# Performance work log

Measured on AMD Instinct MI355X. Metric: run time of the kernel, lower is better.

The kernel has to match this reference:

```python
import jax, jax.numpy as jnp
import numpy as np

B, S, D, DFF = 4, 2048, 1024, 4096
EPS = 1e-5


def layernorm(x, gamma, beta):
    mu = jnp.mean(x, axis=-1, keepdims=True)
    var = jnp.var(x, axis=-1, keepdims=True)
    return (x - mu) * jax.lax.rsqrt(var + EPS) * gamma + beta


def attention(Q, K, V, causal):
    d_k = Q.shape[-1]
    scores = jnp.einsum('bqd,bkd->bqk', Q, K) / jnp.sqrt(jnp.asarray(d_k, Q.dtype))
    if causal:
        q_len, k_len = scores.shape[-2], scores.shape[-1]
        mask = jnp.tril(jnp.ones((q_len, k_len), dtype=bool))
        scores = jnp.where(mask[None], scores, jnp.asarray(-jnp.inf, scores.dtype))
    w = jax.nn.softmax(scores, axis=-1)
    return jnp.einsum('bqk,bkd->bqd', w, V)


def setup_inputs() -> dict:
    key = jax.random.key(0)
    ks = jax.random.split(key, 12)
    sd = 0.02
    return {
        'y': jax.random.normal(ks[0], (B, S, D), jnp.float32),
        'Z': jax.random.normal(ks[1], (B, S, D), jnp.float32),
        'w1': jax.random.normal(ks[2], (D, DFF), jnp.float32) * sd,
        'b1': jnp.zeros((DFF,), jnp.float32),
        'w2': jax.random.normal(ks[3], (DFF, D), jnp.float32) * sd,
        'b2': jnp.zeros((D,), jnp.float32),
        'g1': jnp.ones((D,), jnp.float32), 'beta1': jnp.zeros((D,), jnp.float32),
        'g2': jnp.ones((D,), jnp.float32), 'beta2': jnp.zeros((D,), jnp.float32),
        'g3': jnp.ones((D,), jnp.float32), 'beta3': jnp.zeros((D,), jnp.float32),
    }


def reference(y, Z, w1, b1, w2, b2, g1, beta1, g2, beta2, g3, beta3):
    # masked (causal) self-attention, single head over full d_model
    sa = attention(y, y, y, causal=True)
    y = layernorm(y + sa, g1, beta1)
    # cross-attention to encoder memory Z
    ca = attention(y, Z, Z, causal=False)
    y = layernorm(y + ca, g2, beta2)
    # position-wise FFN
    h = jax.nn.relu(jnp.einsum('bsd,df->bsf', y, w1) + b1)
    ff = jnp.einsum('bsf,fd->bsd', h, w2) + b2
    y = layernorm(y + ff, g3, beta3)
    return y
```

## Files before the change

kernel.cpp:

```cpp
#include <hip/hip_runtime.h>
#include <hip/hip_bf16.h>


#define Bb 4
#define Ss 2048
#define Dd 1024
#define Ff 4096

typedef __attribute__((ext_vector_type(4))) float f32x4;
typedef __attribute__((ext_vector_type(8))) short bf16x8;
typedef __attribute__((ext_vector_type(8))) unsigned short u16x8;
typedef __attribute__((ext_vector_type(4))) unsigned short u16x4;

__device__ __forceinline__ unsigned short f2bf(float f) {
  unsigned u = __float_as_uint(f);
  u += 0x7FFFu + ((u >> 16) & 1u);
  return (unsigned short)(u >> 16);
}

__device__ __forceinline__ void gload_lds16(const void* g, void* l) {
  __builtin_amdgcn_global_load_lds((const __attribute__((address_space(1))) void*)g,
                                   (__attribute__((address_space(3))) void*)l, 16, 0, 0);
}

__device__ __forceinline__ int xcd8(int orig, int n) {
  int q = n >> 3, r = n & 7;
  int x = orig & 7;
  int base = x < r ? x * (q + 1) : r * (q + 1) + (x - r) * q;
  return base + (orig >> 3);
}

__global__ __launch_bounds__(256) void k_transpose_cast(const float* __restrict__ in,
                                                        unsigned short* __restrict__ outT,
                                                        unsigned short* __restrict__ outR,
                                                        int R, int C) {
  __shared__ float t[32][33];
  size_t bo = (size_t)blockIdx.z * R * C;
  const float* pin = in + bo;
  unsigned short* poutT = outT + bo;
  unsigned short* poutR = outR ? outR + bo : nullptr;
  int c0 = blockIdx.x * 32, r0 = blockIdx.y * 32;
  int tx = threadIdx.x, ty = threadIdx.y;
#pragma unroll
  for (int i = 0; i < 4; i++) {
    float v = pin[(size_t)(r0 + ty + i * 8) * C + c0 + tx];
    t[ty + i * 8][tx] = v;
    if (poutR) poutR[(size_t)(r0 + ty + i * 8) * C + c0 + tx] = f2bf(v);
  }
  __syncthreads();
#pragma unroll
  for (int i = 0; i < 4; i++)
    poutT[(size_t)(c0 + ty + i * 8) * R + r0 + tx] = f2bf(t[tx][ty + i * 8]);
}

#define BAR() __builtin_amdgcn_s_barrier()
#define PRIO1() __builtin_amdgcn_s_setprio(1)
#define PRIO0() __builtin_amdgcn_s_setprio(0)

#define LDA8(arr, mh, bo)                                                       \
  {                                                                             \
    _Pragma("unroll") for (int j_ = 0; j_ < QM; ++j_) {                         \
      _Pragma("unroll") for (int kh_ = 0; kh_ < 2; ++kh_) {                     \
        arr[j_][kh_] =                                                          \
            *(const bf16x8*)(lds + (bo) + ((mh)*QM + j_) * 2048 + aof[kh_]);    \
      }                                                                         \
    }                                                                           \
  }

#define LDB8(arr, nh, bo)                                                       \
  {                                                                             \
    _Pragma("unroll") for (int n_ = 0; n_ < 2; ++n_) {                          \
      _Pragma("unroll") for (int kh_ = 0; kh_ < 2; ++kh_) {                     \
        arr[n_][kh_] =                                                          \
            *(const bf16x8*)(lds + (bo) + ((nh)*2 + n_) * 2048 + bof[kh_]);     \
      }                                                                         \
    }                                                                           \
  }

#define MMQ(aarr, barr, mh, nh)                                                 \
  {                                                                             \
    _Pragma("unroll") for (int j_ = 0; j_ < QM; ++j_) {                         \
      _Pragma("unroll") for (int n_ = 0; n_ < 2; ++n_) {                        \
        _Pragma("unroll") for (int kh_ = 0; kh_ < 2; ++kh_) {                   \
          acc[(mh)*QM + j_][(nh)*2 + n_] = __builtin_amdgcn_mfma_f32_16x16x32_bf16( \
              aarr[j_][kh_], barr[n_][kh_], acc[(mh)*QM + j_][(nh)*2 + n_], 0, 0, 0); \
        }                                                                       \
      }                                                                         \
    }                                                                           \
  }

#define VMCNT()                                                                 \
  {                                                                             \
    if constexpr (NVM == 6) asm volatile("s_waitcnt vmcnt(6)" ::: "memory");    \
    else asm volatile("s_waitcnt vmcnt(4)" ::: "memory");                       \
  }

template <int BMt, int EPI, bool CAUSAL, bool KCAP>
__global__ __launch_bounds__(512) void k_gemm8(
    const unsigned short* __restrict__ Ag, const unsigned short* __restrict__ Bg,
    float* __restrict__ Cf, unsigned short* __restrict__ Cb,
    const float* __restrict__ bias, int K, int lda, int ldb, int ldc,
    long bsA, long bsB, long bsC, float scale) {
  constexpr int BNt = 256;
  constexpr int WMS = BMt / 2;
  constexpr int MR = WMS / 16;
  constexpr int QM = MR / 2;
  constexpr int LA = BMt / 128;
  constexpr int NVM = 2 * LA + 2;
  constexpr int ABYTES = BMt * 128;
  constexpr int BBYTES = BNt * 128;
  __shared__ alignas(16) char lds[2 * ABYTES + 2 * BBYTES];

  int i0, j0;
  if (CAUSAL) {
    int t = xcd8(blockIdx.x, gridDim.x);
    int ti = (int)((sqrtf(8.f * t + 1.f) - 1.f) * 0.5f);
    while ((ti + 1) * (ti + 2) / 2 <= t) ++ti;
    while (ti * (ti + 1) / 2 > t) --ti;
    i0 = ti * BMt;
    j0 = (t - ti * (ti + 1) / 2) * BNt;
  } else {
    int lin = xcd8(blockIdx.y * gridDim.x + blockIdx.x, gridDim.x * gridDim.y);
    i0 = (lin / gridDim.x) * BMt;
    j0 = (lin % gridDim.x) * BNt;
  }
  int bz = blockIdx.z;
  Ag += (size_t)bz * bsA;
  Bg += (size_t)bz * bsB;

  int nk = K / 64;
  if (KCAP) {
    int cap = i0 / 64 + BMt / 64;
    nk = nk < cap ? nk : cap;
  }
  const int niter = nk / 2;

  const int tid = threadIdx.x;
  const int w = tid >> 6, lane = tid & 63;
  const int wr = w >> 2, wc = w & 3;

  const int srow = (w << 3) + (lane >> 3);
  const int bcs = (lane & 7) ^ (lane >> 3);
  const unsigned short* As = Ag + (size_t)(i0 + srow) * lda + bcs * 8;
  const unsigned short* Bs = Bg + (size_t)(j0 + srow) * ldb + bcs * 8;
  char* ldsAw = lds + w * 1024;
  char* ldsBw = lds + 2 * ABYTES + w * 1024;

  auto stA = [&](int kt, int hf) {
    int ks = kt < nk ? kt : nk - 1;
#pragma unroll
    for (int l = 0; l < LA; ++l)
      gload_lds16(As + (size_t)(hf * (BMt / 2) + l * 64) * lda + ks * 64,
                  ldsAw + (kt & 1) * ABYTES + hf * (BMt / 2) * 128 + l * 8192);
  };
  auto stB = [&](int kt, int hf) {
    int ks = kt < nk ? kt : nk - 1;
#pragma unroll
    for (int l = 0; l < 2; ++l)
      gload_lds16(Bs + (size_t)(hf * 128 + l * 64) * ldb + ks * 64,
                  ldsBw + (kt & 1) * BBYTES + hf * 128 * 128 + l * 8192);
  };

  const int fr = lane & 15, kq = lane >> 4;
  const int rA = wr * WMS + fr;
  const int rB = wc * 64 + fr;
  unsigned aof[2], bof[2];
  aof[0] = rA * 128 + ((kq ^ (rA & 7)) << 4);
  aof[1] = rA * 128 + (((kq + 4) ^ (rA & 7)) << 4);
  bof[0] = 2 * ABYTES + rB * 128 + ((kq ^ (rB & 7)) << 4);
  bof[1] = 2 * ABYTES + rB * 128 + (((kq + 4) ^ (rB & 7)) << 4);
  constexpr int A0 = 0, A1 = ABYTES, B0 = 0, B1 = BBYTES;

  f32x4 acc[MR][4];
#pragma unroll
  for (int m = 0; m < MR; ++m)
#pragma unroll
    for (int n = 0; n < 4; ++n) acc[m][n] = (f32x4){0.f, 0.f, 0.f, 0.f};

  bf16x8 a0[QM][2], a1[QM][2], b0[2][2], b1[2][2];

  stA(0, 0); stA(0, 1); stB(0, 0); stB(0, 1);
  stA(1, 0); stA(1, 1); stB(1, 0);
  VMCNT();
  BAR();

  for (int t = 0; t < niter; ++t) {
    const int ka = 2 * t + 2, kb = 2 * t + 3;
    LDA8(a0, 0, A0); LDB8(b0, 0, B0);
    stB(2 * t + 1, 1);
    BAR(); PRIO1(); MMQ(a0, b0, 0, 0); PRIO0(); BAR();
    LDA8(a1, 1, A0);
    BAR(); PRIO1(); MMQ(a1, b0, 1, 0); PRIO0(); BAR();
    LDB8(b1, 1, B0);
    stA(ka, 0);
    BAR(); PRIO1(); MMQ(a1, b1, 1, 1); PRIO0(); BAR();
    stA(ka, 1); stB(ka, 0);
    VMCNT();
    BAR(); PRIO1(); MMQ(a0, b1, 0, 1); PRIO0(); BAR();
    LDA8(a0, 0, A1); LDB8(b0, 0, B1);
    stB(ka, 1);
    BAR(); PRIO1(); MMQ(a0, b0, 0, 0); PRIO0(); BAR();
    LDA8(a1, 1, A1);
    BAR(); PRIO1(); MMQ(a1, b0, 1, 0); PRIO0(); BAR();
    LDB8(b1, 1, B1);
    stA(kb, 0);
    BAR(); PRIO1(); MMQ(a1, b1, 1, 1); PRIO0(); BAR();
    stA(kb, 1); stB(kb, 0);
    VMCNT();
    BAR(); PRIO1(); MMQ(a0, b1, 0, 1); PRIO0(); BAR();
  }

  const int colb = j0 + wc * 64 + fr;
  const int rowb = i0 + wr * WMS + (kq << 2);
  const size_t cb = (size_t)bz * bsC;
#pragma unroll
  for (int m = 0; m < MR; ++m) {
#pragma unroll
    for (int r = 0; r < 4; ++r) {
      size_t ro = cb + (size_t)(rowb + m * 16 + r) * ldc;
#pragma unroll
      for (int n = 0; n < 4; ++n) {
        float v = acc[m][n][r];
        int col = colb + n * 16;
        if (EPI == 0) Cf[ro + col] = v * scale;
        else if (EPI == 1) Cf[ro + col] = v;
        else if (EPI == 2) Cb[ro + col] = f2bf(fmaxf(v + bias[col], 0.f));
        else Cf[ro + col] = v + bias[col];
      }
    }
  }
}

template <bool CAUSAL>
__global__ __launch_bounds__(256) void k_softmax(float* __restrict__ scores) {
  int row = blockIdx.x;
  int i = row & (Ss - 1);
  float* src = scores + (size_t)row * Ss;
  unsigned short* dst = (unsigned short*)src;
  int nv = CAUSAL ? i + 1 : Ss;
  int t = threadIdx.x;
  int w = t >> 6, lane = t & 63;
  float v[8];
  float mx = -1e30f;
#pragma unroll
  for (int k = 0; k < 8; k++) {
    int j = t + k * 256;
    v[k] = (j < nv) ? src[j] : -1e30f;
    mx = fmaxf(mx, v[k]);
  }
#pragma unroll
  for (int o = 32; o; o >>= 1) mx = fmaxf(mx, __shfl_xor(mx, o));
  __shared__ float red[8];
  if (lane == 0) red[w] = mx;
  __syncthreads();
  mx = fmaxf(fmaxf(red[0], red[1]), fmaxf(red[2], red[3]));
  float sum = 0.f;
#pragma unroll
  for (int k = 0; k < 8; k++) {
    int j = t + k * 256;
    float e = (j < nv) ? __expf(v[k] - mx) : 0.f;
    v[k] = e;
    sum += e;
  }
#pragma unroll
  for (int o = 32; o; o >>= 1) sum += __shfl_xor(sum, o);
  if (lane == 0) red[4 + w] = sum;
  __syncthreads();
  sum = red[4] + red[5] + red[6] + red[7];
  float inv = 1.f / sum;
#pragma unroll
  for (int k = 0; k < 8; k++) {
    int j = t + k * 256;
    dst[j] = f2bf(v[k] * inv);
  }
}

__global__ __launch_bounds__(256) void k_add_ln(const float* __restrict__ a,
                                                const float* __restrict__ b,
                                                const float* __restrict__ g,
                                                const float* __restrict__ be,
                                                float* __restrict__ outf,
                                                unsigned short* __restrict__ outb) {
  int row = blockIdx.x;
  size_t o = (size_t)row * Dd;
  int t = threadIdx.x;
  f32x4 xa = *(const f32x4*)(a + o + t * 4);
  f32x4 xb = *(const f32x4*)(b + o + t * 4);
  f32x4 x = xa + xb;
  float s = x[0] + x[1] + x[2] + x[3];
  float q = x[0] * x[0] + x[1] * x[1] + x[2] * x[2] + x[3] * x[3];
  int w = t >> 6, lane = t & 63;
#pragma unroll
  for (int of = 32; of; of >>= 1) {
    s += __shfl_xor(s, of);
    q += __shfl_xor(q, of);
  }
  __shared__ float red[8];
  if (lane == 0) {
    red[w] = s;
    red[4 + w] = q;
  }
  __syncthreads();
  s = red[0] + red[1] + red[2] + red[3];
  q = red[4] + red[5] + red[6] + red[7];
  float mean = s * (1.f / Dd);
  float var = q * (1.f / Dd) - mean * mean;
  float rstd = rsqrtf(var + 1e-5f);
  f32x4 gv = *(const f32x4*)(g + t * 4);
  f32x4 bv = *(const f32x4*)(be + t * 4);
  f32x4 y;
#pragma unroll
  for (int k = 0; k < 4; k++) y[k] = (x[k] - mean) * rstd * gv[k] + bv[k];
  *(f32x4*)(outf + o + t * 4) = y;
  if (outb) {
    u16x4 r;
    r[0] = f2bf(y[0]); r[1] = f2bf(y[1]); r[2] = f2bf(y[2]); r[3] = f2bf(y[3]);
    *(u16x4*)(outb + o + t * 4) = r;
  }
}

extern "C" void kernel_launch(void* const* d_in, const int* in_sizes, int n_in, void* d_out,
                              int out_size, void* d_ws, size_t ws_size, hipStream_t stream) {
  (void)in_sizes; (void)n_in; (void)out_size; (void)ws_size;
  const float* y   = (const float*)d_in[0];
  const float* Z   = (const float*)d_in[1];
  const float* w1  = (const float*)d_in[2];
  const float* b1  = (const float*)d_in[3];
  const float* w2  = (const float*)d_in[4];
  const float* b2  = (const float*)d_in[5];
  const float* g1  = (const float*)d_in[6];
  const float* be1 = (const float*)d_in[7];
  const float* g2  = (const float*)d_in[8];
  const float* be2 = (const float*)d_in[9];
  const float* g3  = (const float*)d_in[10];
  const float* be3 = (const float*)d_in[11];
  float* out = (float*)d_out;

  char* ws = (char*)d_ws;
  const size_t MB = 1024ull * 1024ull;
  unsigned short* T   = (unsigned short*)(ws);
  unsigned short* Zbf = (unsigned short*)(ws + 16 * MB);
  unsigned short* ybf = (unsigned short*)(ws + 32 * MB);
  unsigned short* w1t = (unsigned short*)(ws + 48 * MB);
  unsigned short* w2t = (unsigned short*)(ws + 56 * MB);
  float* sc           = (float*)(ws + 64 * MB);
  unsigned short* h   = (unsigned short*)(ws + 64 * MB);
  float* res          = (float*)(ws + 128 * MB);
  float* attn         = (float*)d_out;

  dim3 b256(256), b512(512);
  const float scl = 1.f / 32.f;

  k_transpose_cast<<<dim3(Dd / 32, Ss / 32, Bb), dim3(32, 8), 0, stream>>>(y, T, ybf, Ss, Dd);
  k_gemm8<256, 0, true, false><<<dim3(36, 1, Bb), b512, 0, stream>>>(
      ybf, ybf, sc, nullptr, nullptr, Dd, Dd, Dd, Ss, (long)Ss * Dd, (long)Ss * Dd,
      (long)Ss * Ss, scl);
  k_softmax<true><<<dim3(Bb * Ss), b256, 0, stream>>>(sc);
  k_gemm8<128, 1, false, true><<<dim3(Dd / 256, Ss / 128, Bb), b512, 0, stream>>>(
      (const unsigned short*)sc, T, attn, nullptr, nullptr, Ss, 2 * Ss, Ss, Dd,
      2L * Ss * Ss, (long)Dd * Ss, (long)Ss * Dd, 1.f);
  k_add_ln<<<dim3(Bb * Ss), b256, 0, stream>>>(y, attn, g1, be1, res, ybf);

  k_transpose_cast<<<dim3(Dd / 32, Ss / 32, Bb), dim3(32, 8), 0, stream>>>(Z, T, Zbf, Ss, Dd);
  k_gemm8<256, 0, false, false><<<dim3(Ss / 256, Ss / 256, Bb), b512, 0, stream>>>(
      ybf, Zbf, sc, nullptr, nullptr, Dd, Dd, Dd, Ss, (long)Ss * Dd, (long)Ss * Dd,
      (long)Ss * Ss, scl);
  k_softmax<false><<<dim3(Bb * Ss), b256, 0, stream>>>(sc);
  k_gemm8<128, 1, false, false><<<dim3(Dd / 256, Ss / 128, Bb), b512, 0, stream>>>(
      (const unsigned short*)sc, T, attn, nullptr, nullptr, Ss, 2 * Ss, Ss, Dd,
      2L * Ss * Ss, (long)Dd * Ss, (long)Ss * Dd, 1.f);
  k_add_ln<<<dim3(Bb * Ss), b256, 0, stream>>>(res, attn, g2, be2, res, ybf);

  k_transpose_cast<<<dim3(Ff / 32, Dd / 32, 1), dim3(32, 8), 0, stream>>>(w1, w1t, nullptr, Dd, Ff);
  k_transpose_cast<<<dim3(Dd / 32, Ff / 32, 1), dim3(32, 8), 0, stream>>>(w2, w2t, nullptr, Ff, Dd);
  k_gemm8<256, 2, false, false><<<dim3(Ff / 256, (Bb * Ss) / 256, 1), b512, 0, stream>>>(
      ybf, w1t, nullptr, h, b1, Dd, Dd, Dd, Ff, 0L, 0L, 0L, 1.f);
  k_gemm8<128, 3, false, false><<<dim3(Dd / 256, (Bb * Ss) / 128, 1), b512, 0, stream>>>(
      h, w2t, attn, nullptr, b2, Ff, Ff, Ff, Dd, 0L, 0L, 0L, 1.f);
  k_add_ln<<<dim3(Bb * Ss), b256, 0, stream>>>(res, attn, g3, be3, out, nullptr);
}
```

Measured before the change: 406.5 us.

## Write attention scores as bf16, vectorize softmax, split GEMM into 256/128-row kernels

The score GEMMs now write bf16 scores directly instead of fp32. The softmax reads and writes those bf16 values in place with 8-wide vector accesses. This halves score-matrix traffic in the QK GEMM store and the softmax read. The old templated GEMM is split into a 256-row kernel and a dedicated 128-row kernel with its own load pipeline, and explicit lgkmcnt waits are added before each MFMA phase. The risks are extra bf16 rounding before the max and exp in softmax, and more conservative waits that could reduce LDS/MFMA overlap.

```diff
diff --git a/kernel.cpp b/kernel.cpp
--- a/kernel.cpp
+++ b/kernel.cpp
@@ -16,6 +16,9 @@
   unsigned u = __float_as_uint(f);
   u += 0x7FFFu + ((u >> 16) & 1u);
   return (unsigned short)(u >> 16);
+}
+__device__ __forceinline__ float bf2f(unsigned short h) {
+  return __uint_as_float(((unsigned)h) << 16);
 }
 
 __device__ __forceinline__ void gload_lds16(const void* g, void* l) {
@@ -56,6 +59,11 @@
 #define BAR() __builtin_amdgcn_s_barrier()
 #define PRIO1() __builtin_amdgcn_s_setprio(1)
 #define PRIO0() __builtin_amdgcn_s_setprio(0)
+#define LGKM0()                                          \
+  {                                                      \
+    asm volatile("s_waitcnt lgkmcnt(0)" ::: "memory");   \
+    __builtin_amdgcn_sched_barrier(0);                   \
+  }
 
 #define LDA8(arr, mh, bo)                                                       \
   {                                                                             \
@@ -89,26 +97,34 @@
     }                                                                           \
   }
 
-#define VMCNT()                                                                 \
+#define EPILOGUE(MR_, WMS_)                                                     \
   {                                                                             \
-    if constexpr (NVM == 6) asm volatile("s_waitcnt vmcnt(6)" ::: "memory");    \
-    else asm volatile("s_waitcnt vmcnt(4)" ::: "memory");                       \
-  }
-
-template <int BMt, int EPI, bool CAUSAL, bool KCAP>
+    const int colb = j0 + wc * 64 + fr;                                         \
+    const int rowb = i0 + wr * (WMS_) + (kq << 2);                              \
+    const size_t cb = (size_t)bz * bsC;                                         \
+    _Pragma("unroll") for (int m = 0; m < (MR_); ++m) {                         \
+      _Pragma("unroll") for (int r = 0; r < 4; ++r) {                           \
+        size_t ro = cb + (size_t)(rowb + m * 16 + r) * ldc;                     \
+        _Pragma("unroll") for (int n = 0; n < 4; ++n) {                         \
+          float v = acc[m][n][r];                                               \
+          int col = colb + n * 16;                                              \
+          if (EPI == 0) Cb[ro + col] = f2bf(v * scale);                         \
+          else if (EPI == 1) Cf[ro + col] = v;                                  \
+          else if (EPI == 2) Cb[ro + col] = f2bf(fmaxf(v + bias[col], 0.f));    \
+          else Cf[ro + col] = v + bias[col];                                    \
+        }                                                                       \
+      }                                                                         \
+    }                                                                           \
+  }
+
+template <int EPI, bool CAUSAL>
 __global__ __launch_bounds__(512) void k_gemm8(
     const unsigned short* __restrict__ Ag, const unsigned short* __restrict__ Bg,
     float* __restrict__ Cf, unsigned short* __restrict__ Cb,
     const float* __restrict__ bias, int K, int lda, int ldb, int ldc,
     long bsA, long bsB, long bsC, float scale) {
-  constexpr int BNt = 256;
-  constexpr int WMS = BMt / 2;
-  constexpr int MR = WMS / 16;
-  constexpr int QM = MR / 2;
-  constexpr int LA = BMt / 128;
-  constexpr int NVM = 2 * LA + 2;
-  constexpr int ABYTES = BMt * 128;
-  constexpr int BBYTES = BNt * 128;
+  constexpr int QM = 4;
+  constexpr int ABYTES = 32768, BBYTES = 32768;
   __shared__ alignas(16) char lds[2 * ABYTES + 2 * BBYTES];
 
   int i0, j0;
@@ -117,22 +133,18 @@
     int ti = (int)((sqrtf(8.f * t + 1.f) - 1.f) * 0.5f);
     while ((ti + 1) * (ti + 2) / 2 <= t) ++ti;
     while (ti * (ti + 1) / 2 > t) --ti;
-    i0 = ti * BMt;
-    j0 = (t - ti * (ti + 1) / 2) * BNt;
+    i0 = ti * 256;
+    j0 = (t - ti * (ti + 1) / 2) * 256;
   } else {
     int lin = xcd8(blockIdx.y * gridDim.x + blockIdx.x, gridDim.x * gridDim.y);
-    i0 = (lin / gridDim.x) * BMt;
-    j0 = (lin % gridDim.x) * BNt;
+    i0 = (lin / gridDim.x) * 256;
+    j0 = (lin % gridDim.x) * 256;
   }
   int bz = blockIdx.z;
   Ag += (size_t)bz * bsA;
   Bg += (size_t)bz * bsB;
 
-  int nk = K / 64;
-  if (KCAP) {
-    int cap = i0 / 64 + BMt / 64;
-    nk = nk < cap ? nk : cap;
-  }
+  const int nk = K / 64;
   const int niter = nk / 2;
 
   const int tid = threadIdx.x;
@@ -149,9 +161,9 @@
   auto stA = [&](int kt, int hf) {
     int ks = kt < nk ? kt : nk - 1;
 #pragma unroll
-    for (int l = 0; l < LA; ++l)
-      gload_lds16(As + (size_t)(hf * (BMt / 2) + l * 64) * lda + ks * 64,
-                  ldsAw + (kt & 1) * ABYTES + hf * (BMt / 2) * 128 + l * 8192);
+    for (int l = 0; l < 2; ++l)
+      gload_lds16(As + (size_t)(hf * 128 + l * 64) * lda + ks * 64,
+                  ldsAw + (kt & 1) * ABYTES + hf * 128 * 128 + l * 8192);
   };
   auto stB = [&](int kt, int hf) {
     int ks = kt < nk ? kt : nk - 1;
@@ -162,7 +174,7 @@
   };
 
   const int fr = lane & 15, kq = lane >> 4;
-  const int rA = wr * WMS + fr;
+  const int rA = wr * 128 + fr;
   const int rB = wc * 64 + fr;
   unsigned aof[2], bof[2];
   aof[0] = rA * 128 + ((kq ^ (rA & 7)) << 4);
@@ -171,9 +183,9 @@
   bof[1] = 2 * ABYTES + rB * 128 + (((kq + 4) ^ (rB & 7)) << 4);
   constexpr int A0 = 0, A1 = ABYTES, B0 = 0, B1 = BBYTES;
 
-  f32x4 acc[MR][4];
-#pragma unroll
-  for (int m = 0; m < MR; ++m)
+  f32x4 acc[8][4];
+#pragma unroll
+  for (int m = 0; m < 8; ++m)
 #pragma unroll
     for (int n = 0; n < 4; ++n) acc[m][n] = (f32x4){0.f, 0.f, 0.f, 0.f};
 
@@ -181,71 +193,146 @@
 
   stA(0, 0); stA(0, 1); stB(0, 0); stB(0, 1);
   stA(1, 0); stA(1, 1); stB(1, 0);
-  VMCNT();
+  asm volatile("s_waitcnt vmcnt(6)" ::: "memory");
   BAR();
 
   for (int t = 0; t < niter; ++t) {
     const int ka = 2 * t + 2, kb = 2 * t + 3;
     LDA8(a0, 0, A0); LDB8(b0, 0, B0);
     stB(2 * t + 1, 1);
-    BAR(); PRIO1(); MMQ(a0, b0, 0, 0); PRIO0(); BAR();
+    BAR(); LGKM0(); PRIO1(); MMQ(a0, b0, 0, 0); PRIO0(); BAR();
     LDA8(a1, 1, A0);
-    BAR(); PRIO1(); MMQ(a1, b0, 1, 0); PRIO0(); BAR();
+    BAR(); LGKM0(); PRIO1(); MMQ(a1, b0, 1, 0); PRIO0(); BAR();
     LDB8(b1, 1, B0);
     stA(ka, 0);
-    BAR(); PRIO1(); MMQ(a1, b1, 1, 1); PRIO0(); BAR();
+    BAR(); LGKM0(); PRIO1(); MMQ(a1, b1, 1, 1); PRIO0(); BAR();
     stA(ka, 1); stB(ka, 0);
-    VMCNT();
+    asm volatile("s_waitcnt vmcnt(6)" ::: "memory");
     BAR(); PRIO1(); MMQ(a0, b1, 0, 1); PRIO0(); BAR();
     LDA8(a0, 0, A1); LDB8(b0, 0, B1);
     stB(ka, 1);
-    BAR(); PRIO1(); MMQ(a0, b0, 0, 0); PRIO0(); BAR();
+    BAR(); LGKM0(); PRIO1(); MMQ(a0, b0, 0, 0); PRIO0(); BAR();
     LDA8(a1, 1, A1);
-    BAR(); PRIO1(); MMQ(a1, b0, 1, 0); PRIO0(); BAR();
+    BAR(); LGKM0(); PRIO1(); MMQ(a1, b0, 1, 0); PRIO0(); BAR();
     LDB8(b1, 1, B1);
     stA(kb, 0);
-    BAR(); PRIO1(); MMQ(a1, b1, 1, 1); PRIO0(); BAR();
+    BAR(); LGKM0(); PRIO1(); MMQ(a1, b1, 1, 1); PRIO0(); BAR();
     stA(kb, 1); stB(kb, 0);
-    VMCNT();
+    asm volatile("s_waitcnt vmcnt(6)" ::: "memory");
     BAR(); PRIO1(); MMQ(a0, b1, 0, 1); PRIO0(); BAR();
   }
-
-  const int colb = j0 + wc * 64 + fr;
-  const int rowb = i0 + wr * WMS + (kq << 2);
-  const size_t cb = (size_t)bz * bsC;
-#pragma unroll
-  for (int m = 0; m < MR; ++m) {
-#pragma unroll
-    for (int r = 0; r < 4; ++r) {
-      size_t ro = cb + (size_t)(rowb + m * 16 + r) * ldc;
-#pragma unroll
-      for (int n = 0; n < 4; ++n) {
-        float v = acc[m][n][r];
-        int col = colb + n * 16;
-        if (EPI == 0) Cf[ro + col] = v * scale;
-        else if (EPI == 1) Cf[ro + col] = v;
-        else if (EPI == 2) Cb[ro + col] = f2bf(fmaxf(v + bias[col], 0.f));
-        else Cf[ro + col] = v + bias[col];
-      }
-    }
-  }
+  EPILOGUE(8, 128)
+}
+
+template <int EPI, bool KCAP>
+__global__ __launch_bounds__(512) void k_gemm4(
+    const unsigned short* __restrict__ Ag, const unsigned short* __restrict__ Bg,
+    float* __restrict__ Cf, unsigned short* __restrict__ Cb,
+    const float* __restrict__ bias, int K, int lda, int ldb, int ldc,
+    long bsA, long bsB, long bsC, float scale) {
+  constexpr int QM = 4;
+  constexpr int ABYTES = 16384, BBYTES = 32768;
+  __shared__ alignas(16) char lds[2 * ABYTES + 2 * BBYTES];
+
+  int lin = xcd8(blockIdx.y * gridDim.x + blockIdx.x, gridDim.x * gridDim.y);
+  int i0 = (lin / gridDim.x) * 128;
+  int j0 = (lin % gridDim.x) * 256;
+  int bz = blockIdx.z;
+  Ag += (size_t)bz * bsA;
+  Bg += (size_t)bz * bsB;
+
+  int nk = K / 64;
+  if (KCAP) {
+    int cap = i0 / 64 + 2;
+    nk = nk < cap ? nk : cap;
+  }
+  const int niter = nk / 2;
+
+  const int tid = threadIdx.x;
+  const int w = tid >> 6, lane = tid & 63;
+  const int wr = w >> 2, wc = w & 3;
+
+  const int srow = (w << 3) + (lane >> 3);
+  const int bcs = (lane & 7) ^ (lane >> 3);
+  const unsigned short* As = Ag + (size_t)(i0 + srow) * lda + bcs * 8;
+  const unsigned short* Bs = Bg + (size_t)(j0 + srow) * ldb + bcs * 8;
+  char* ldsAw = lds + w * 1024;
+  char* ldsBw = lds + 2 * ABYTES + w * 1024;
+
+  auto stA2 = [&](int kt) {
+    int ks = kt < nk ? kt : nk - 1;
+#pragma unroll
+    for (int hf = 0; hf < 2; ++hf)
+      gload_lds16(As + (size_t)(hf * 64) * lda + ks * 64,
+                  ldsAw + (kt & 1) * ABYTES + hf * 64 * 128);
+  };
+  auto stB2 = [&](int kt) {
+    int ks = kt < nk ? kt : nk - 1;
+#pragma unroll
+    for (int hf = 0; hf < 2; ++hf)
+#pragma unroll
+      for (int l = 0; l < 2; ++l)
+        gload_lds16(Bs + (size_t)(hf * 128 + l * 64) * ldb + ks * 64,
+                    ldsBw + (kt & 1) * BBYTES + hf * 128 * 128 + l * 8192);
+  };
+
+  const int fr = lane & 15, kq = lane >> 4;
+  const int rA = wr * 64 + fr;
+  const int rB = wc * 64 + fr;
+  unsigned aof[2], bof[2];
+  aof[0] = rA * 128 + ((kq ^ (rA & 7)) << 4);
+  aof[1] = rA * 128 + (((kq + 4) ^ (rA & 7)) << 4);
+  bof[0] = 2 * ABYTES + rB * 128 + ((kq ^ (rB & 7)) << 4);
+  bof[1] = 2 * ABYTES + rB * 128 + (((kq + 4) ^ (rB & 7)) << 4);
+  constexpr int A0 = 0, A1 = ABYTES, B0 = 0, B1 = BBYTES;
+
+  f32x4 acc[4][4];
+#pragma unroll
+  for (int m = 0; m < 4; ++m)
+#pragma unroll
+    for (int n = 0; n < 4; ++n) acc[m][n] = (f32x4){0.f, 0.f, 0.f, 0.f};
+
+  bf16x8 a[QM][2], b0[2][2], b1[2][2];
+
+  stA2(0); stB2(0); stA2(1);
+  asm volatile("s_waitcnt vmcnt(2)" ::: "memory");
+  BAR();
+
+  for (int t = 0; t < niter; ++t) {
+    const int ka = 2 * t + 2, kb = 2 * t + 3;
+    LDA8(a, 0, A0); LDB8(b0, 0, B0);
+    stB2(2 * t + 1);
+    BAR(); LGKM0(); PRIO1(); MMQ(a, b0, 0, 0); PRIO0(); BAR();
+    LDB8(b1, 1, B0);
+    stA2(ka);
+    asm volatile("s_waitcnt vmcnt(2)" ::: "memory");
+    BAR(); LGKM0(); PRIO1(); MMQ(a, b1, 0, 1); PRIO0(); BAR();
+    LDA8(a, 0, A1); LDB8(b0, 0, B1);
+    stB2(ka);
+    BAR(); LGKM0(); PRIO1(); MMQ(a, b0, 0, 0); PRIO0(); BAR();
+    LDB8(b1, 1, B1);
+    stA2(kb);
+    asm volatile("s_waitcnt vmcnt(2)" ::: "memory");
+    BAR(); LGKM0(); PRIO1(); MMQ(a, b1, 0, 1); PRIO0(); BAR();
+  }
+  EPILOGUE(4, 64)
 }
 
 template <bool CAUSAL>
-__global__ __launch_bounds__(256) void k_softmax(float* __restrict__ scores) {
+__global__ __launch_bounds__(256) void k_softmax(unsigned short* __restrict__ scores) {
   int row = blockIdx.x;
   int i = row & (Ss - 1);
-  float* src = scores + (size_t)row * Ss;
-  unsigned short* dst = (unsigned short*)src;
+  unsigned short* src = scores + (size_t)row * Ss;
   int nv = CAUSAL ? i + 1 : Ss;
   int t = threadIdx.x;
   int w = t >> 6, lane = t & 63;
+  u16x8 raw = *(const u16x8*)(src + t * 8);
   float v[8];
   float mx = -1e30f;
 #pragma unroll
   for (int k = 0; k < 8; k++) {
-    int j = t + k * 256;
-    v[k] = (j < nv) ? src[j] : -1e30f;
+    int j = t * 8 + k;
+    v[k] = (j < nv) ? bf2f(raw[k]) : -1e30f;
     mx = fmaxf(mx, v[k]);
   }
 #pragma unroll
@@ -257,7 +344,7 @@
   float sum = 0.f;
 #pragma unroll
   for (int k = 0; k < 8; k++) {
-    int j = t + k * 256;
+    int j = t * 8 + k;
     float e = (j < nv) ? __expf(v[k] - mx) : 0.f;
     v[k] = e;
     sum += e;
@@ -268,11 +355,10 @@
   __syncthreads();
   sum = red[4] + red[5] + red[6] + red[7];
   float inv = 1.f / sum;
-#pragma unroll
-  for (int k = 0; k < 8; k++) {
-    int j = t + k * 256;
-    dst[j] = f2bf(v[k] * inv);
-  }
+  u16x8 r;
+#pragma unroll
+  for (int k = 0; k < 8; k++) r[k] = f2bf(v[k] * inv);
+  *(u16x8*)(src + t * 8) = r;
 }
 
 __global__ __launch_bounds__(256) void k_add_ln(const float* __restrict__ a,
@@ -343,7 +429,7 @@
   unsigned short* ybf = (unsigned short*)(ws + 32 * MB);
   unsigned short* w1t = (unsigned short*)(ws + 48 * MB);
   unsigned short* w2t = (unsigned short*)(ws + 56 * MB);
-  float* sc           = (float*)(ws + 64 * MB);
+  unsigned short* sc  = (unsigned short*)(ws + 64 * MB);
   unsigned short* h   = (unsigned short*)(ws + 64 * MB);
   float* res          = (float*)(ws + 128 * MB);
   float* attn         = (float*)d_out;
@@ -352,30 +438,30 @@
   const float scl = 1.f / 32.f;
 
   k_transpose_cast<<<dim3(Dd / 32, Ss / 32, Bb), dim3(32, 8), 0, stream>>>(y, T, ybf, Ss, Dd);
-  k_gemm8<256, 0, true, false><<<dim3(36, 1, Bb), b512, 0, stream>>>(
-      ybf, ybf, sc, nullptr, nullptr, Dd, Dd, Dd, Ss, (long)Ss * Dd, (long)Ss * Dd,
+  k_gemm8<0, true><<<dim3(36, 1, Bb), b512, 0, stream>>>(
+      ybf, ybf, nullptr, sc, nullptr, Dd, Dd, Dd, Ss, (long)Ss * Dd, (long)Ss * Dd,
       (long)Ss * Ss, scl);
   k_softmax<true><<<dim3(Bb * Ss), b256, 0, stream>>>(sc);
-  k_gemm8<128, 1, false, true><<<dim3(Dd / 256, Ss / 128, Bb), b512, 0, stream>>>(
-      (const unsigned short*)sc, T, attn, nullptr, nullptr, Ss, 2 * Ss, Ss, Dd,
-      2L * Ss * Ss, (long)Dd * Ss, (long)Ss * Dd, 1.f);
+  k_gemm4<1, true><<<dim3(Dd / 256, Ss / 128, Bb), b512, 0, stream>>>(
+      sc, T, attn, nullptr, nullptr, Ss, Ss, Ss, Dd,
+      (long)Ss * Ss, (long)Dd * Ss, (long)Ss * Dd, 1.f);
   k_add_ln<<<dim3(Bb * Ss), b256, 0, stream>>>(y, attn, g1, be1, res, ybf);
 
   k_transpose_cast<<<dim3(Dd / 32, Ss / 32, Bb), dim3(32, 8), 0, stream>>>(Z, T, Zbf, Ss, Dd);
-  k_gemm8<256, 0, false, false><<<dim3(Ss / 256, Ss / 256, Bb), b512, 0, stream>>>(
-      ybf, Zbf, sc, nullptr, nullptr, Dd, Dd, Dd, Ss, (long)Ss * Dd, (long)Ss * Dd,
+  k_gemm8<0, false><<<dim3(Ss / 256, Ss / 256, Bb), b512, 0, stream>>>(
+      ybf, Zbf, nullptr, sc, nullptr, Dd, Dd, Dd, Ss, (long)Ss * Dd, (long)Ss * Dd,
       (long)Ss * Ss, scl);
   k_softmax<false><<<dim3(Bb * Ss), b256, 0, stream>>>(sc);
-  k_gemm8<128, 1, false, false><<<dim3(Dd / 256, Ss / 128, Bb), b512, 0, stream>>>(
-      (const unsigned short*)sc, T, attn, nullptr, nullptr, Ss, 2 * Ss, Ss, Dd,
-      2L * Ss * Ss, (long)Dd * Ss, (long)Ss * Dd, 1.f);
+  k_gemm4<1, false><<<dim3(Dd / 256, Ss / 128, Bb), b512, 0, stream>>>(
+      sc, T, attn, nullptr, nullptr, Ss, Ss, Ss, Dd,
+      (long)Ss * Ss, (long)Dd * Ss, (long)Ss * Dd, 1.f);
   k_add_ln<<<dim3(Bb * Ss), b256, 0, stream>>>(res, attn, g2, be2, res, ybf);
 
   k_transpose_cast<<<dim3(Ff / 32, Dd / 32, 1), dim3(32, 8), 0, stream>>>(w1, w1t, nullptr, Dd, Ff);
   k_transpose_cast<<<dim3(Dd / 32, Ff / 32, 1), dim3(32, 8), 0, stream>>>(w2, w2t, nullptr, Ff, Dd);
-  k_gemm8<256, 2, false, false><<<dim3(Ff / 256, (Bb * Ss) / 256, 1), b512, 0, stream>>>(
+  k_gemm8<2, false><<<dim3(Ff / 256, (Bb * Ss) / 256, 1), b512, 0, stream>>>(
       ybf, w1t, nullptr, h, b1, Dd, Dd, Dd, Ff, 0L, 0L, 0L, 1.f);
-  k_gemm8<128, 3, false, false><<<dim3(Dd / 256, (Bb * Ss) / 128, 1), b512, 0, stream>>>(
+  k_gemm4<3, false><<<dim3(Dd / 256, (Bb * Ss) / 128, 1), b512, 0, stream>>>(
       h, w2t, attn, nullptr, b2, Ff, Ff, Ff, Dd, 0L, 0L, 0L, 1.f);
   k_add_ln<<<dim3(Bb * Ss), b256, 0, stream>>>(res, attn, g3, be3, out, nullptr);
 }
```

Result: no change. 403.4 us (-0.8%).
